# Kernel optimization log

Measured on AMD Instinct MI355X. Metric: run time of the kernel, lower is better.

The kernel has to match this reference:

```python
import jax, jax.numpy as jnp
import numpy as np
from jax import lax

B, S = 16, 512
H = 512          # hidden_size == embedding_dim (required by the module's own wiring)
V = 10000        # dict_len
G = 4 * H


def setup_inputs() -> dict:
    key = jax.random.key(0)
    ks = jax.random.split(key, 16)
    sc = 0.05
    inp = {
        "source": jax.random.randint(ks[0], (B, S), 0, V),
        "w_emb": jax.random.normal(ks[1], (H, V), jnp.float32) * sc,
        "b_emb": jax.random.normal(ks[2], (H,), jnp.float32) * sc,
        "w_ih0": jax.random.normal(ks[3], (G, H), jnp.float32) * sc,
        "w_hh0": jax.random.normal(ks[4], (G, H), jnp.float32) * sc,
        "b_ih0": jax.random.normal(ks[5], (G,), jnp.float32) * sc,
        "b_hh0": jax.random.normal(ks[6], (G,), jnp.float32) * sc,
        "w_ih1": jax.random.normal(ks[7], (G, H), jnp.float32) * sc,
        "w_hh1": jax.random.normal(ks[8], (G, H), jnp.float32) * sc,
        "b_ih1": jax.random.normal(ks[9], (G,), jnp.float32) * sc,
        "b_hh1": jax.random.normal(ks[10], (G,), jnp.float32) * sc,
        "w1": jax.random.normal(ks[11], (128, H), jnp.float32) * sc,
        "b1": jax.random.normal(ks[12], (128,), jnp.float32) * sc,
        "w2": jax.random.normal(ks[13], (V, 128), jnp.float32) * sc,
        "b2": jax.random.normal(ks[14], (V,), jnp.float32) * sc,
    }
    return inp


def _lstm_layer(x, w_ih, w_hh, b_ih, b_hh):
    # x: [B, S, H] -> hs: [B, S, H]; PyTorch gate order i, f, g, o
    b, s, _ = x.shape
    h_dim = w_hh.shape[1]
    # precompute input projections for all timesteps
    x_proj = jnp.einsum('bsd,gd->bsg', x, w_ih) + b_ih + b_hh  # [B, S, 4H]

    def step(carry, xt):
        h, c = carry
        gates = xt + h @ w_hh.T                      # [B, 4H]
        i, f, g, o = jnp.split(gates, 4, axis=-1)
        i = jax.nn.sigmoid(i)
        f = jax.nn.sigmoid(f)
        g = jnp.tanh(g)
        o = jax.nn.sigmoid(o)
        c = f * c + i * g
        h = o * jnp.tanh(c)
        return (h, c), h

    h0 = jnp.zeros((b, h_dim), x.dtype)
    c0 = jnp.zeros((b, h_dim), x.dtype)
    _, hs = lax.scan(step, (h0, c0), jnp.swapaxes(x_proj, 0, 1))  # [S, B, H]
    return jnp.swapaxes(hs, 0, 1)


def reference(source, w_emb, b_emb,
              w_ih0, w_hh0, b_ih0, b_hh0,
              w_ih1, w_hh1, b_ih1, b_hh1,
              w1, b1, w2, b2):
    # one_hot(source) @ w_emb.T + b_emb == row-gather of w_emb.T (identical math)
    emb = jnp.take(w_emb.T, source, axis=0) + b_emb        # [B, S, H]
    h = _lstm_layer(emb, w_ih0, w_hh0, b_ih0, b_hh0)
    h = _lstm_layer(h, w_ih1, w_hh1, b_ih1, b_hh1)         # dropout identity at eval
    hid = jax.nn.relu(jnp.einsum('bsh,kh->bsk', h, w1) + b1)  # [B, S, 128]
    logits = jnp.einsum('bsk,vk->bsv', hid, w2) + b2       # [B, S, V]
    return logits
```

## Files before the change

kernel.cpp:

```cpp
#include <hip/hip_runtime.h>
#include <hip/hip_bf16.h>

#define B_ 16
#define S_ 512
#define H_ 512
#define V_ 10000
#define G_ 2048
#define M_ (B_*S_)

typedef short bf16x8 __attribute__((ext_vector_type(8)));
typedef float f32x4 __attribute__((ext_vector_type(4)));
typedef _Float16 f16x8 __attribute__((ext_vector_type(8)));

static __device__ __forceinline__ unsigned short f2bf(float x) {
    union { float f; unsigned int u; } v; v.f = x;
    unsigned int r = v.u + 0x7fffu + ((v.u >> 16) & 1u);
    return (unsigned short)(r >> 16);
}
static __device__ __forceinline__ unsigned short f2h_bits(float x) {
    _Float16 h = (_Float16)x;
    return __builtin_bit_cast(unsigned short, h);
}

__global__ void prep_kernel(const float* __restrict__ w_ih0, const float* __restrict__ w_hh0,
                            const float* __restrict__ b_ih0, const float* __restrict__ b_hh0,
                            const float* __restrict__ w_ih1, const float* __restrict__ w_hh1,
                            const float* __restrict__ b_ih1, const float* __restrict__ b_hh1,
                            const float* __restrict__ w1,   const float* __restrict__ w2,
                            unsigned short* __restrict__ w_ih0_b, _Float16* __restrict__ wfrag0,
                            _Float16* __restrict__ wfrag1x,      _Float16* __restrict__ wfrag1h,
                            unsigned short* __restrict__ w1_b,    unsigned short* __restrict__ w2_b,
                            float* __restrict__ bias0, float* __restrict__ bias1) {
    int i  = blockIdx.x * blockDim.x + threadIdx.x;
    int st = gridDim.x * blockDim.x;
    for (int k = i; k < G_*H_; k += st) w_ih0_b[k] = f2bf(w_ih0[k]);
    for (int d = i; d < G_*H_; d += st) {
        int e    = d & 7;
        int l    = (d >> 3) & 63;
        int wrow = (d >> 9) & 7;
        int kc   = (d >> 12) & 15;
        int j    = (d >> 16) & 15;
        int r    = wrow*16 + (l & 15);
        int R    = (r >> 5)*512 + j*32 + (r & 31);
        int k    = kc*32 + ((l >> 4) << 3) + e;
        wfrag0[d] = (_Float16)w_hh0[R*H_ + k];
    }
    for (int d = i; d < G_*H_; d += st) {
        int e    = d & 7;
        int l    = (d >> 3) & 63;
        int nt   = (d >> 9) & 1;
        int kc   = (d >> 10) & 15;
        int j    = (d >> 14) & 63;
        int r    = nt*16 + (l & 15);
        int R    = (r >> 3)*512 + j*8 + (r & 7);
        int k    = kc*32 + ((l >> 4) << 3) + e;
        wfrag1x[d] = (_Float16)w_ih1[R*H_ + k];
        wfrag1h[d] = (_Float16)w_hh1[R*H_ + k];
    }
    for (int k = i; k < V_*128; k += st) w2_b[k] = f2bf(w2[k]);
    for (int k = i; k < 128*H_; k += st) w1_b[k] = f2bf(w1[k]);
    for (int k = i; k < G_;     k += st) { bias0[k] = b_ih0[k] + b_hh0[k]; bias1[k] = b_ih1[k] + b_hh1[k]; }
}

__global__ void embed_kernel(const int* __restrict__ src, const float* __restrict__ w_emb,
                             const float* __restrict__ b_emb, unsigned short* __restrict__ emb) {
    int m = blockIdx.x;
    int idx = src[m];
    for (int h = threadIdx.x; h < H_; h += blockDim.x)
        emb[(long)m*H_ + h] = f2bf(w_emb[(long)h*V_ + idx] + b_emb[h]);
}

template<bool RELU, bool OUT_BF16>
__launch_bounds__(256)
__global__ void gemm_kernel(const unsigned short* __restrict__ A, const unsigned short* __restrict__ Bm,
                            const float* __restrict__ bias, void* __restrict__ Cout,
                            int Ndim, int K) {
    __shared__ unsigned short At[128*40];
    __shared__ unsigned short Bt[128*40];
    int m0 = blockIdx.y * 128;
    int n0 = blockIdx.x * 128;
    int tid  = threadIdx.x;
    int lane = tid & 63, wave = tid >> 6;
    int wm = (wave >> 1) * 64, wn = (wave & 1) * 64;
    int l15 = lane & 15, l4 = lane >> 4;
    f32x4 acc[4][4] = {};

    for (int kk = 0; kk < K; kk += 32) {
        __syncthreads();
        #pragma unroll
        for (int rep = 0; rep < 2; ++rep) {
            int gid = tid + rep*256;
            int row = gid >> 2, c8 = (gid & 3) << 3;
            *(uint4*)&At[row*40 + c8] = *(const uint4*)&A[(long)(m0+row)*K + kk + c8];
            int nrow = n0 + row; if (nrow >= Ndim) nrow = Ndim - 1;
            *(uint4*)&Bt[row*40 + c8] = *(const uint4*)&Bm[(long)nrow*K + kk + c8];
        }
        __syncthreads();
        bf16x8 af[4], bfr[4];
        #pragma unroll
        for (int i = 0; i < 4; ++i)
            af[i] = *(const bf16x8*)&At[(wm + i*16 + l15)*40 + l4*8];
        #pragma unroll
        for (int j = 0; j < 4; ++j)
            bfr[j] = *(const bf16x8*)&Bt[(wn + j*16 + l15)*40 + l4*8];
        #pragma unroll
        for (int i = 0; i < 4; ++i)
            #pragma unroll
            for (int j = 0; j < 4; ++j)
                acc[i][j] = __builtin_amdgcn_mfma_f32_16x16x32_bf16(af[i], bfr[j], acc[i][j], 0, 0, 0);
    }

    #pragma unroll
    for (int i = 0; i < 4; ++i) {
        int row = m0 + wm + i*16 + l4*4;
        #pragma unroll
        for (int j = 0; j < 4; ++j) {
            int col = n0 + wn + j*16 + l15;
            if (col < Ndim) {
                float bv = bias[col];
                #pragma unroll
                for (int r = 0; r < 4; ++r) {
                    float v = acc[i][j][r] + bv;
                    if (RELU) v = v > 0.f ? v : 0.f;
                    if (OUT_BF16) ((unsigned short*)Cout)[(long)(row+r)*Ndim + col] = f2bf(v);
                    else          ((float*)Cout)[(long)(row+r)*Ndim + col] = v;
                }
            }
        }
    }
}

__launch_bounds__(512)
__global__ void lstm_fused_kernel(const float* __restrict__ xp,
                                  const uint4* __restrict__ wfrag0,
                                  const uint4* __restrict__ wfrag1x,
                                  const uint4* __restrict__ wfrag1h,
                                  const float* __restrict__ bias1,
                                  unsigned long long* __restrict__ h0ex,
                                  unsigned long long* __restrict__ h1ex,
                                  unsigned short* __restrict__ hout) {
    __shared__ __align__(16) char smem[156160];
    int tid  = threadIdx.x;
    int lane = tid & 63, wave = tid >> 6;
    int l15  = lane & 15, l4 = lane >> 4;

    if (blockIdx.x < 16) {
        uint4*     w_lds = (uint4*)smem;
        _Float16*  h_lds = (_Float16*)(smem + 131072);
        float*     gbuf  = (float*)(smem + 131072 + 16640);
        int j = blockIdx.x;
        for (int i = tid; i < 8192; i += 512) w_lds[i] = wfrag0[(long)j*8192 + i];
        for (int i = tid; i < 4160; i += 512) ((unsigned int*)h_lds)[i] = 0;
        __syncthreads();
        const _Float16* wh = (const _Float16*)w_lds;
        int ch = tid >> 5, s = tid & 31;
        float c = 0.f;

        for (int t = 0; t < S_; ++t) {
            const float* xr = xp + ((long)ch*S_ + t)*G_ + j*32 + s;
            float xi = xr[0], xf = xr[512], xg = xr[1024], xo = xr[1536];
            if (t > 0) {
                unsigned int tagv = (unsigned int)t;
                const unsigned long long* base = h0ex + (long)(t-1)*4096;
                unsigned long long v[8];
                for (;;) {
                    #pragma unroll
                    for (int q = 0; q < 8; ++q)
                        v[q] = __hip_atomic_load(base + q*512 + tid, __ATOMIC_RELAXED, __HIP_MEMORY_SCOPE_AGENT);
                    bool ok = true;
                    #pragma unroll
                    for (int q = 0; q < 8; ++q)
                        ok &= ((unsigned int)(v[q] >> 32) == tagv);
                    if (ok) break;
                    __builtin_amdgcn_s_sleep(1);
                }
                #pragma unroll
                for (int q = 0; q < 8; ++q) {
                    int w = q*512 + tid;
                    *(unsigned int*)&h_lds[(w >> 8)*520 + (w & 255)*2] = (unsigned int)v[q];
                }
            }
            __syncthreads();
            f32x4 acc = {0.f,0.f,0.f,0.f};
            #pragma unroll
            for (int kc = 0; kc < 16; ++kc) {
                f16x8 af = *(const f16x8*)&h_lds[l15*520 + kc*32 + l4*8];
                f16x8 bf = *(const f16x8*)&wh[(((kc*8) + wave)*64 + lane)*8];
                acc = __builtin_amdgcn_mfma_f32_16x16x32_f16(af, bf, acc, 0, 0, 0);
            }
            #pragma unroll
            for (int r = 0; r < 4; ++r)
                gbuf[(l4*4 + r)*132 + wave*16 + l15] = acc[r];
            __syncthreads();
            const float* gb = gbuf + ch*132;
            xi += gb[s]; xf += gb[32+s]; xg += gb[64+s]; xo += gb[96+s];
            float ig = 1.f/(1.f+__expf(-xi));
            float fg = 1.f/(1.f+__expf(-xf));
            float gg = tanhf(xg);
            float og = 1.f/(1.f+__expf(-xo));
            c = fg*c + ig*gg;
            float h = og*tanhf(c);
            unsigned int me = f2h_bits(h);
            unsigned int up = (unsigned int)__shfl_down((int)me, 1, 64);
            if (!(s & 1)) {
                unsigned long long vv = ((unsigned long long)(unsigned int)(t+1) << 32)
                                      | (up << 16) | me;
                __hip_atomic_store(&h0ex[(long)t*4096 + ch*256 + j*16 + (s>>1)], vv,
                                   __ATOMIC_RELAXED, __HIP_MEMORY_SCOPE_AGENT);
            }
        }
    } else {
        uint4*     wx   = (uint4*)smem;
        uint4*     whh  = wx + 2048;
        _Float16*  h0l  = (_Float16*)(smem + 65536);
        _Float16*  h1l  = h0l + 16*520;
        float*     gbuf = (float*)(smem + 65536 + 2*16640);
        float*     bl   = gbuf + 2*2*16*36;
        int j1 = blockIdx.x - 16;
        for (int i = tid; i < 2048; i += 512) {
            wx[i]  = wfrag1x[(long)j1*2048 + i];
            whh[i] = wfrag1h[(long)j1*2048 + i];
        }
        if (tid < 32) bl[tid] = bias1[(tid >> 3)*512 + j1*8 + (tid & 7)];
        for (int i = tid; i < 8320; i += 512) ((unsigned int*)h0l)[i] = 0;
        __syncthreads();
        int ch = tid >> 3, sc = tid & 7;
        float c = 0.f;

        for (int t = 0; t < S_; ++t) {
            {
                unsigned int tag0 = (unsigned int)(t+1);
                unsigned int tag1 = (unsigned int)t;
                const unsigned long long* b0 = h0ex + (long)t*4096;
                const unsigned long long* b1 = h1ex + (long)(t > 0 ? t-1 : 0)*4096;
                unsigned long long v0[8], v1[8];
                for (;;) {
                    #pragma unroll
                    for (int q = 0; q < 8; ++q)
                        v0[q] = __hip_atomic_load(b0 + q*512 + tid, __ATOMIC_RELAXED, __HIP_MEMORY_SCOPE_AGENT);
                    if (t > 0) {
                        #pragma unroll
                        for (int q = 0; q < 8; ++q)
                            v1[q] = __hip_atomic_load(b1 + q*512 + tid, __ATOMIC_RELAXED, __HIP_MEMORY_SCOPE_AGENT);
                    }
                    bool ok = true;
                    #pragma unroll
                    for (int q = 0; q < 8; ++q)
                        ok &= ((unsigned int)(v0[q] >> 32) == tag0);
                    if (t > 0) {
                        #pragma unroll
                        for (int q = 0; q < 8; ++q)
                            ok &= ((unsigned int)(v1[q] >> 32) == tag1);
                    }
                    if (ok) break;
                    __builtin_amdgcn_s_sleep(1);
                }
                if (t > 0) {
                    #pragma unroll
                    for (int q = 0; q < 8; ++q) {
                        int w = q*512 + tid;
                        *(unsigned int*)&h1l[(w >> 8)*520 + (w & 255)*2] = (unsigned int)v1[q];
                    }
                }
                #pragma unroll
                for (int q = 0; q < 8; ++q) {
                    int w = q*512 + tid;
                    *(unsigned int*)&h0l[(w >> 8)*520 + (w & 255)*2] = (unsigned int)v0[q];
                }
            }
            __syncthreads();
            {
                int src = wave >> 2, nt = (wave >> 1) & 1, kh = wave & 1;
                const _Float16* hs = src ? h1l : h0l;
                const _Float16* ws = (const _Float16*)(src ? whh : wx);
                f32x4 acc = {0.f,0.f,0.f,0.f};
                #pragma unroll
                for (int k2 = 0; k2 < 8; ++k2) {
                    int kc = kh*8 + k2;
                    f16x8 af = *(const f16x8*)&hs[l15*520 + kc*32 + l4*8];
                    f16x8 bf = *(const f16x8*)&ws[((kc*2 + nt)*64 + lane)*8];
                    acc = __builtin_amdgcn_mfma_f32_16x16x32_f16(af, bf, acc, 0, 0, 0);
                }
                #pragma unroll
                for (int r = 0; r < 4; ++r)
                    gbuf[((src*2 + kh)*16 + (l4*4 + r))*36 + nt*16 + l15] = acc[r];
            }
            __syncthreads();
            if (tid < 128) {
                const float* g0 = gbuf + (0*16 + ch)*36;
                const float* g1 = gbuf + (1*16 + ch)*36;
                const float* g2 = gbuf + (2*16 + ch)*36;
                const float* g3 = gbuf + (3*16 + ch)*36;
                float xi = g0[sc]    + g1[sc]    + g2[sc]    + g3[sc]    + bl[sc];
                float xf = g0[8+sc]  + g1[8+sc]  + g2[8+sc]  + g3[8+sc]  + bl[8+sc];
                float xg = g0[16+sc] + g1[16+sc] + g2[16+sc] + g3[16+sc] + bl[16+sc];
                float xo = g0[24+sc] + g1[24+sc] + g2[24+sc] + g3[24+sc] + bl[24+sc];
                float ig = 1.f/(1.f+__expf(-xi));
                float fg = 1.f/(1.f+__expf(-xf));
                float gg = tanhf(xg);
                float og = 1.f/(1.f+__expf(-xo));
                c = fg*c + ig*gg;
                float h = og*tanhf(c);
                hout[((long)ch*S_ + t)*H_ + j1*8 + sc] = f2bf(h);
                unsigned int me = f2h_bits(h);
                unsigned int up = (unsigned int)__shfl_down((int)me, 1, 64);
                if (!(sc & 1)) {
                    unsigned long long vv = ((unsigned long long)(unsigned int)(t+1) << 32)
                                          | (up << 16) | me;
                    __hip_atomic_store(&h1ex[(long)t*4096 + ch*256 + j1*4 + (sc>>1)], vv,
                                       __ATOMIC_RELAXED, __HIP_MEMORY_SCOPE_AGENT);
                }
            }
        }
    }
}

extern "C" void kernel_launch(void* const* d_in, const int* in_sizes, int n_in,
                              void* d_out, int out_size, void* d_ws, size_t ws_size,
                              hipStream_t stream) {
    const int*   src   = (const int*)  d_in[0];
    const float* w_emb = (const float*)d_in[1];
    const float* b_emb = (const float*)d_in[2];
    const float* w_ih0 = (const float*)d_in[3];
    const float* w_hh0 = (const float*)d_in[4];
    const float* b_ih0 = (const float*)d_in[5];
    const float* b_hh0 = (const float*)d_in[6];
    const float* w_ih1 = (const float*)d_in[7];
    const float* w_hh1 = (const float*)d_in[8];
    const float* b_ih1 = (const float*)d_in[9];
    const float* b_hh1 = (const float*)d_in[10];
    const float* w1    = (const float*)d_in[11];
    const float* b1    = (const float*)d_in[12];
    const float* w2    = (const float*)d_in[13];
    const float* b2    = (const float*)d_in[14];
    float* out = (float*)d_out;

    char* ws = (char*)d_ws;
    size_t off = 0;
    auto alloc = [&](size_t bytes) -> void* {
        void* p = ws + off;
        off = (off + bytes + 255) & ~(size_t)255;
        return p;
    };
    unsigned short* w_ih0_b = (unsigned short*)alloc((size_t)G_*H_*2);
    _Float16*       wfrag0  = (_Float16*)      alloc((size_t)G_*H_*2);
    _Float16*       wfrag1x = (_Float16*)      alloc((size_t)G_*H_*2);
    _Float16*       wfrag1h = (_Float16*)      alloc((size_t)G_*H_*2);
    unsigned short* w1_b    = (unsigned short*)alloc((size_t)128*H_*2);
    unsigned short* w2_b    = (unsigned short*)alloc((size_t)V_*128*2);
    float*          bias0   = (float*)         alloc((size_t)G_*4);
    float*          bias1   = (float*)         alloc((size_t)G_*4);
    unsigned short* emb     = (unsigned short*)alloc((size_t)M_*H_*2);
    unsigned short* hidb    = (unsigned short*)alloc((size_t)M_*128*2);
    float*          xp      = (float*)         alloc((size_t)M_*G_*4);
    unsigned long long* h0ex = (unsigned long long*)alloc((size_t)S_*4096*8);
    unsigned long long* h1ex = (unsigned long long*)alloc((size_t)S_*4096*8);

    prep_kernel<<<2048, 256, 0, stream>>>(w_ih0, w_hh0, b_ih0, b_hh0,
                                          w_ih1, w_hh1, b_ih1, b_hh1,
                                          w1, w2,
                                          w_ih0_b, wfrag0, wfrag1x, wfrag1h,
                                          w1_b, w2_b, bias0, bias1);
    embed_kernel<<<M_, 256, 0, stream>>>(src, w_emb, b_emb, emb);

    gemm_kernel<false,false><<<dim3(G_/128, M_/128), 256, 0, stream>>>(emb, w_ih0_b, bias0, xp, G_, H_);

    lstm_fused_kernel<<<80, 512, 0, stream>>>(xp, (const uint4*)wfrag0,
                                              (const uint4*)wfrag1x, (const uint4*)wfrag1h,
                                              bias1, h0ex, h1ex, emb);

    gemm_kernel<true,true><<<dim3(1, M_/128), 256, 0, stream>>>(emb, w1_b, b1, hidb, 128, H_);

    gemm_kernel<false,false><<<dim3((V_+127)/128, M_/128), 256, 0, stream>>>(hidb, w2_b, b2, out, V_, 128);
}
```

Baseline: 2.433 ms.

## Use ring buffers for LSTM hidden-state exchange with per-launch tags and backpressure

Shrinks the per-timestep hidden-state exchange buffers from full S-length arrays to small ring buffers (16 slots for layer 0, 4 for layer 1). Correctness is kept by tagging entries with a per-launch epoch counter and making layer-0 blocks periodically wait on layer-1 progress counters. It also swaps tanhf for an exp-based fast tanh. The aim is a smaller working set that stays in cache and cheaper gate math, at the cost of extra backpressure synchronisation that could stall layer 0.

```diff
diff --git a/kernel.cpp b/kernel.cpp
--- a/kernel.cpp
+++ b/kernel.cpp
@@ -20,6 +20,12 @@
 static __device__ __forceinline__ unsigned short f2h_bits(float x) {
     _Float16 h = (_Float16)x;
     return __builtin_bit_cast(unsigned short, h);
+}
+static __device__ __forceinline__ float ftanh(float x) {
+    float ax = fabsf(x);
+    float e  = __expf(-2.f*ax);
+    float r  = (1.f - e) / (1.f + e);
+    return copysignf(r, x);
 }
 
 __global__ void prep_kernel(const float* __restrict__ w_ih0, const float* __restrict__ w_hh0,
@@ -30,7 +36,10 @@
                             unsigned short* __restrict__ w_ih0_b, _Float16* __restrict__ wfrag0,
                             _Float16* __restrict__ wfrag1x,      _Float16* __restrict__ wfrag1h,
                             unsigned short* __restrict__ w1_b,    unsigned short* __restrict__ w2_b,
-                            float* __restrict__ bias0, float* __restrict__ bias1) {
+                            float* __restrict__ bias0, float* __restrict__ bias1,
+                            unsigned int* __restrict__ l1prog, unsigned int* __restrict__ lc_slot) {
+    if (blockIdx.x == 0 && threadIdx.x == 0) atomicAdd(lc_slot, 1u);
+    if (blockIdx.x == 0 && threadIdx.x < 64) l1prog[threadIdx.x*16] = 0u;
     int i  = blockIdx.x * blockDim.x + threadIdx.x;
     int st = gridDim.x * blockDim.x;
     for (int k = i; k < G_*H_; k += st) w_ih0_b[k] = f2bf(w_ih0[k]);
@@ -138,11 +147,14 @@
                                   const float* __restrict__ bias1,
                                   unsigned long long* __restrict__ h0ex,
                                   unsigned long long* __restrict__ h1ex,
+                                  unsigned int* __restrict__ l1prog,
+                                  const unsigned int* __restrict__ lc_slot,
                                   unsigned short* __restrict__ hout) {
     __shared__ __align__(16) char smem[156160];
     int tid  = threadIdx.x;
     int lane = tid & 63, wave = tid >> 6;
     int l15  = lane & 15, l4 = lane >> 4;
+    unsigned int base = __hip_atomic_load(lc_slot, __ATOMIC_RELAXED, __HIP_MEMORY_SCOPE_AGENT) << 16;
 
     if (blockIdx.x < 16) {
         uint4*     w_lds = (uint4*)smem;
@@ -159,14 +171,22 @@
         for (int t = 0; t < S_; ++t) {
             const float* xr = xp + ((long)ch*S_ + t)*G_ + j*32 + s;
             float xi = xr[0], xf = xr[512], xg = xr[1024], xo = xr[1536];
+            if (wave == 0 && t >= 16 && (t & 7) == 0) {
+                unsigned int thr = base + (unsigned int)(t - 8);
+                unsigned int pv = __hip_atomic_load(l1prog + lane*16, __ATOMIC_RELAXED, __HIP_MEMORY_SCOPE_AGENT);
+                while (!__all((int)(pv >= thr))) {
+                    __builtin_amdgcn_s_sleep(4);
+                    pv = __hip_atomic_load(l1prog + lane*16, __ATOMIC_RELAXED, __HIP_MEMORY_SCOPE_AGENT);
+                }
+            }
             if (t > 0) {
-                unsigned int tagv = (unsigned int)t;
-                const unsigned long long* base = h0ex + (long)(t-1)*4096;
+                unsigned int tagv = base + (unsigned int)t;
+                const unsigned long long* bse = h0ex + (long)((t-1) & 15)*4096;
                 unsigned long long v[8];
                 for (;;) {
                     #pragma unroll
                     for (int q = 0; q < 8; ++q)
-                        v[q] = __hip_atomic_load(base + q*512 + tid, __ATOMIC_RELAXED, __HIP_MEMORY_SCOPE_AGENT);
+                        v[q] = __hip_atomic_load(bse + q*512 + tid, __ATOMIC_RELAXED, __HIP_MEMORY_SCOPE_AGENT);
                     bool ok = true;
                     #pragma unroll
                     for (int q = 0; q < 8; ++q)
@@ -196,16 +216,16 @@
             xi += gb[s]; xf += gb[32+s]; xg += gb[64+s]; xo += gb[96+s];
             float ig = 1.f/(1.f+__expf(-xi));
             float fg = 1.f/(1.f+__expf(-xf));
-            float gg = tanhf(xg);
+            float gg = ftanh(xg);
             float og = 1.f/(1.f+__expf(-xo));
             c = fg*c + ig*gg;
-            float h = og*tanhf(c);
+            float h = og*ftanh(c);
             unsigned int me = f2h_bits(h);
             unsigned int up = (unsigned int)__shfl_down((int)me, 1, 64);
             if (!(s & 1)) {
-                unsigned long long vv = ((unsigned long long)(unsigned int)(t+1) << 32)
+                unsigned long long vv = ((unsigned long long)(base + (unsigned int)(t+1)) << 32)
                                       | (up << 16) | me;
-                __hip_atomic_store(&h0ex[(long)t*4096 + ch*256 + j*16 + (s>>1)], vv,
+                __hip_atomic_store(&h0ex[(long)(t & 15)*4096 + ch*256 + j*16 + (s>>1)], vv,
                                    __ATOMIC_RELAXED, __HIP_MEMORY_SCOPE_AGENT);
             }
         }
@@ -229,10 +249,10 @@
 
         for (int t = 0; t < S_; ++t) {
             {
-                unsigned int tag0 = (unsigned int)(t+1);
-                unsigned int tag1 = (unsigned int)t;
-                const unsigned long long* b0 = h0ex + (long)t*4096;
-                const unsigned long long* b1 = h1ex + (long)(t > 0 ? t-1 : 0)*4096;
+                unsigned int tag0 = base + (unsigned int)(t+1);
+                unsigned int tag1 = base + (unsigned int)t;
+                const unsigned long long* b0 = h0ex + (long)(t & 15)*4096;
+                const unsigned long long* b1 = h1ex + (long)((t > 0 ? t-1 : 0) & 3)*4096;
                 unsigned long long v0[8], v1[8];
                 for (;;) {
                     #pragma unroll
@@ -269,6 +289,9 @@
                 }
             }
             __syncthreads();
+            if (tid == 0)
+                __hip_atomic_store(l1prog + j1*16, base + (unsigned int)t,
+                                   __ATOMIC_RELAXED, __HIP_MEMORY_SCOPE_AGENT);
             {
                 int src = wave >> 2, nt = (wave >> 1) & 1, kh = wave & 1;
                 const _Float16* hs = src ? h1l : h0l;
@@ -297,17 +320,17 @@
                 float xo = g0[24+sc] + g1[24+sc] + g2[24+sc] + g3[24+sc] + bl[24+sc];
                 float ig = 1.f/(1.f+__expf(-xi));
                 float fg = 1.f/(1.f+__expf(-xf));
-                float gg = tanhf(xg);
+                float gg = ftanh(xg);
                 float og = 1.f/(1.f+__expf(-xo));
                 c = fg*c + ig*gg;
-                float h = og*tanhf(c);
+                float h = og*ftanh(c);
                 hout[((long)ch*S_ + t)*H_ + j1*8 + sc] = f2bf(h);
                 unsigned int me = f2h_bits(h);
                 unsigned int up = (unsigned int)__shfl_down((int)me, 1, 64);
                 if (!(sc & 1)) {
-                    unsigned long long vv = ((unsigned long long)(unsigned int)(t+1) << 32)
+                    unsigned long long vv = ((unsigned long long)(base + (unsigned int)(t+1)) << 32)
                                           | (up << 16) | me;
-                    __hip_atomic_store(&h1ex[(long)t*4096 + ch*256 + j1*4 + (sc>>1)], vv,
+                    __hip_atomic_store(&h1ex[(long)(t & 3)*4096 + ch*256 + j1*4 + (sc>>1)], vv,
                                        __ATOMIC_RELAXED, __HIP_MEMORY_SCOPE_AGENT);
                 }
             }
@@ -353,21 +376,24 @@
     unsigned short* emb     = (unsigned short*)alloc((size_t)M_*H_*2);
     unsigned short* hidb    = (unsigned short*)alloc((size_t)M_*128*2);
     float*          xp      = (float*)         alloc((size_t)M_*G_*4);
-    unsigned long long* h0ex = (unsigned long long*)alloc((size_t)S_*4096*8);
-    unsigned long long* h1ex = (unsigned long long*)alloc((size_t)S_*4096*8);
+    unsigned long long* h0ex = (unsigned long long*)alloc((size_t)16*4096*8);
+    unsigned long long* h1ex = (unsigned long long*)alloc((size_t)4*4096*8);
+    unsigned int*   l1prog  = (unsigned int*)  alloc((size_t)64*16*4);
+    unsigned int*   lc_slot = (unsigned int*)  alloc((size_t)256);
 
     prep_kernel<<<2048, 256, 0, stream>>>(w_ih0, w_hh0, b_ih0, b_hh0,
                                           w_ih1, w_hh1, b_ih1, b_hh1,
                                           w1, w2,
                                           w_ih0_b, wfrag0, wfrag1x, wfrag1h,
-                                          w1_b, w2_b, bias0, bias1);
+                                          w1_b, w2_b, bias0, bias1,
+                                          l1prog, lc_slot);
     embed_kernel<<<M_, 256, 0, stream>>>(src, w_emb, b_emb, emb);
 
     gemm_kernel<false,false><<<dim3(G_/128, M_/128), 256, 0, stream>>>(emb, w_ih0_b, bias0, xp, G_, H_);
 
     lstm_fused_kernel<<<80, 512, 0, stream>>>(xp, (const uint4*)wfrag0,
                                               (const uint4*)wfrag1x, (const uint4*)wfrag1h,
-                                              bias1, h0ex, h1ex, emb);
+                                              bias1, h0ex, h1ex, l1prog, lc_slot, emb);
 
     gemm_kernel<true,true><<<dim3(1, M_/128), 256, 0, stream>>>(emb, w1_b, b1, hidb, 128, H_);
 
```

Result: no change. 2.458 ms (+1.1%).
